# Performance work log

Hardware: AMD Instinct MI355X
Metric: run time of the kernel (lower is better)

## Reference

```python
import jax, jax.numpy as jnp
import numpy as np

B, N, DIM, H, DH = 4, 2048, 1024, 16, 64

def setup_inputs() -> dict:
    key = jax.random.key(0)
    k1, k2, k3 = jax.random.split(key, 3)
    x = jax.random.normal(k1, (B, N, DIM), dtype=jnp.float32)
    mask = jnp.ones((B, N), dtype=bool)
    w_qkv = jax.random.normal(k2, (DIM, 3 * H * DH), dtype=jnp.float32) * (DIM ** -0.5)
    w_out = jax.random.normal(k3, (H * DH, DIM), dtype=jnp.float32) * ((H * DH) ** -0.5)
    b_out = jnp.zeros((DIM,), dtype=jnp.float32)
    return {"x": x, "mask": mask, "w_qkv": w_qkv, "w_out": w_out, "b_out": b_out}

def reference(x, mask, w_qkv, w_out, b_out):
    b, n, _ = x.shape
    h, dh = H, DH
    scale = dh ** -0.5
    qkv = x @ w_qkv  # [b, n, 3*h*dh]
    q, k, v = jnp.split(qkv, 3, axis=-1)
    # [b, n, h*dh] -> [b, h, n, dh]
    reshape = lambda t: t.reshape(b, n, h, dh).transpose(0, 2, 1, 3)
    q, k, v = reshape(q) * scale, reshape(k), reshape(v)
    dots = jnp.einsum('bhid,bhjd->bhij', q, k)  # materialized N x N scores
    neg = -jnp.finfo(dots.dtype).max
    # key padding mask: [b, j] -> [b, 1, 1, j]
    dots = jnp.where(mask[:, None, None, :], dots, neg)
    # causal mask: mask out j > i
    causal = jnp.triu(jnp.ones((n, n), dtype=bool), k=1)
    dots = jnp.where(causal[None, None, :, :], neg, dots)
    attn = jax.nn.softmax(dots, axis=-1)
    out = jnp.einsum('bhij,bhjd->bhid', attn, v)
    out = out.transpose(0, 2, 1, 3).reshape(b, n, h * dh)
    return out @ w_out + b_out
```

## Files before the change

### kernel.cpp

```cpp
#include <hip/hip_runtime.h>

#define B_   4
#define N_   2048
#define DIM_ 1024
#define H_   16
#define DH_  64
#define NT   (B_ * N_)
#define PS   ((size_t)B_ * H_ * N_ * DH_)

typedef __bf16 bf16x8 __attribute__((ext_vector_type(8)));
typedef short  s16x4  __attribute__((ext_vector_type(4)));
typedef float  f32x4  __attribute__((ext_vector_type(4)));
typedef unsigned int   u32;
typedef unsigned int   u32x2 __attribute__((ext_vector_type(2)));
typedef unsigned short u16;

#define LOG2E 1.44269504088896f
#define QSCALE (0.125f * LOG2E)

__device__ __forceinline__ u16 f2bf(float f) {
  u32 u = __float_as_uint(f);
  u += 0x7FFFu + ((u >> 16) & 1u);
  return (u16)(u >> 16);
}

__device__ __forceinline__ u32 bfpack(float f0, float f1) {
  u32 a = __float_as_uint(f0) + 0x8000u;
  u32 b = __float_as_uint(f1) + 0x8000u;
  return __builtin_amdgcn_perm(b, a, 0x07060302);
}

__device__ __forceinline__ float fexp2(float x) {
  return __builtin_amdgcn_exp2f(x);
}

__device__ __forceinline__ f32x4 mfma32(bf16x8 a, bf16x8 b, f32x4 c) {
  return __builtin_amdgcn_mfma_f32_16x16x32_bf16(a, b, c, 0, 0, 0);
}
__device__ __forceinline__ f32x4 mfma16k(s16x4 a, s16x4 b, f32x4 c) {
  return __builtin_amdgcn_mfma_f32_16x16x16bf16_1k(a, b, c, 0, 0, 0);
}

__device__ __forceinline__ void gld16(const void* g, void* l) {
  __builtin_amdgcn_global_load_lds(
      (const __attribute__((address_space(1))) u32*)g,
      (__attribute__((address_space(3))) u32*)l, 16, 0, 0);
}

__global__ void convert_x_kernel(const float* __restrict__ x, u16* __restrict__ xb) {
  size_t i = ((size_t)blockIdx.x * 256 + threadIdx.x) * 8;
  float4 f0 = *(const float4*)(x + i);
  float4 f1 = *(const float4*)(x + i + 4);
  uint4 o;
  o.x = (u32)f2bf(f0.x) | ((u32)f2bf(f0.y) << 16);
  o.y = (u32)f2bf(f0.z) | ((u32)f2bf(f0.w) << 16);
  o.z = (u32)f2bf(f1.x) | ((u32)f2bf(f1.y) << 16);
  o.w = (u32)f2bf(f1.z) | ((u32)f2bf(f1.w) << 16);
  *(uint4*)(xb + i) = o;
}

__global__ void transpose_conv_kernel(const float* __restrict__ w, u16* __restrict__ wt,
                                      int K, int Ncols) {
  __shared__ u16 T[64 * 66];
  const int n0 = blockIdx.x * 64, k0 = blockIdx.y * 64;
  const int tid = threadIdx.x;
  const int r = tid >> 4, c4 = (tid & 15) * 4;
#pragma unroll
  for (int i = 0; i < 4; ++i) {
    int row = r + i * 16;
    float4 f = *(const float4*)(w + (size_t)(k0 + row) * Ncols + n0 + c4);
    u16* p = &T[row * 66 + c4];
    p[0] = f2bf(f.x); p[1] = f2bf(f.y); p[2] = f2bf(f.z); p[3] = f2bf(f.w);
  }
  __syncthreads();
  const int nr = tid >> 2, kc = (tid & 3) * 16;
  u32 p[8];
#pragma unroll
  for (int j = 0; j < 8; ++j)
    p[j] = (u32)T[(kc + 2 * j) * 66 + nr] | ((u32)T[(kc + 2 * j + 1) * 66 + nr] << 16);
  size_t dst = (size_t)(n0 + nr) * K + k0 + kc;
  *(uint4*)(wt + dst)     = make_uint4(p[0], p[1], p[2], p[3]);
  *(uint4*)(wt + dst + 8) = make_uint4(p[4], p[5], p[6], p[7]);
}

__global__ __launch_bounds__(256) void qkv_gemm_kernel(
    const u16* __restrict__ xb, const u16* __restrict__ wt,
    u16* __restrict__ q, u16* __restrict__ k, u16* __restrict__ vt) {
  __shared__ alignas(16) u16 As[128 * 64];
  __shared__ alignas(16) u16 Bs[128 * 64];
  const int tid = threadIdx.x, wave = tid >> 6, lane = tid & 63;
  const int quad = lane >> 4, l15 = lane & 15;
  const int wm = (wave >> 1) * 64, wn = (wave & 1) * 64;
  const int m0 = blockIdx.y * 128, n0 = blockIdx.x * 128;
  const int srow = lane >> 3;
  const int schunk = (lane & 7) ^ srow;

  f32x4 acc[4][4] = {};

  for (int kt = 0; kt < DIM_; kt += 64) {
    __syncthreads();
#pragma unroll
    for (int i = 0; i < 4; ++i) {
      int c = wave * 4 + i;
      int row = c * 8 + srow;
      gld16(xb + (size_t)(m0 + row) * DIM_ + kt + schunk * 8, As + c * 512);
      gld16(wt + (size_t)(n0 + row) * DIM_ + kt + schunk * 8, Bs + c * 512);
    }
    __syncthreads();
#pragma unroll
    for (int h = 0; h < 2; ++h) {
      bf16x8 af[4], bfr[4];
#pragma unroll
      for (int mi = 0; mi < 4; ++mi) {
        int row = wm + mi * 16 + l15;
        af[mi] = *(const bf16x8*)(As + row * 64 + (((quad + 4 * h) ^ (row & 7)) * 8));
      }
#pragma unroll
      for (int ni = 0; ni < 4; ++ni) {
        int row = wn + ni * 16 + l15;
        bfr[ni] = *(const bf16x8*)(Bs + row * 64 + (((quad + 4 * h) ^ (row & 7)) * 8));
      }
#pragma unroll
      for (int ni = 0; ni < 4; ++ni)
#pragma unroll
        for (int mi = 0; mi < 4; ++mi)
          acc[mi][ni] = mfma32(af[mi], bfr[ni], acc[mi][ni]);
    }
  }

#pragma unroll
  for (int ni = 0; ni < 4; ++ni) {
    int colg = n0 + wn + ni * 16 + l15;
    int part = colg >> 10, rem = colg & 1023;
    int hh = rem >> 6, d = rem & 63;
#pragma unroll
    for (int mi = 0; mi < 4; ++mi) {
      int row0 = m0 + wm + mi * 16 + quad * 4;
      int bb = row0 >> 11, nn0 = row0 & 2047;
      size_t bh = (size_t)(bb * H_ + hh);
      if (part == 0) {
#pragma unroll
        for (int r = 0; r < 4; ++r)
          q[(bh * N_ + nn0 + r) * DH_ + d] = f2bf(acc[mi][ni][r] * QSCALE);
      } else if (part == 1) {
#pragma unroll
        for (int r = 0; r < 4; ++r)
          k[(bh * N_ + nn0 + r) * DH_ + d] = f2bf(acc[mi][ni][r]);
      } else {
        u32 lo = bfpack(acc[mi][ni][0], acc[mi][ni][1]);
        u32 hi = bfpack(acc[mi][ni][2], acc[mi][ni][3]);
        *(uint2*)(vt + (bh * DH_ + d) * N_ + nn0) = make_uint2(lo, hi);
      }
    }
  }
}

__global__ __launch_bounds__(256) void attn_kernel(
    const u16* __restrict__ q, const u16* __restrict__ k,
    const u16* __restrict__ vt, u16* __restrict__ ctx) {
  __shared__ alignas(16) u16 Ks[128 * 64];
  __shared__ alignas(16) u16 Vs[64 * 128];
  const int tid = threadIdx.x, wave = tid >> 6, lane = tid & 63;
  const int quad = lane >> 4, l15 = lane & 15;
  const int head = blockIdx.x;
  const int p = blockIdx.y;
  const int hh = head & 15, bb = head >> 4;
  const int qtr0 = p, qtr1 = 31 - p;

  const size_t bhofs = (size_t)(bb * H_ + hh) << 17;
  const u16* qp = q + bhofs;
  const u16* kp = k + bhofs;
  const u16* vp = vt + bhofs;

  bf16x8 qf[2][2];
#pragma unroll
  for (int rg = 0; rg < 2; ++rg) {
    int rb = (rg ? qtr1 : qtr0) * 64 + wave * 16 + l15;
#pragma unroll
    for (int h = 0; h < 2; ++h)
      qf[rg][h] = *(const bf16x8*)(qp + (size_t)rb * 64 + h * 32 + quad * 8);
  }

  float m_s[2] = {-INFINITY, -INFINITY};
  float l_s[2] = {0.f, 0.f};
  f32x4 o[2][4] = {};

  const int ksrow = lane >> 3;
  const int kschunk = (lane & 7) ^ ksrow;
  const u16* kstage = kp + (size_t)ksrow * 64 + kschunk * 8;
  const int vsrow = lane >> 4;
  const u16* vstage0 = vp + (size_t)vsrow * N_;

  const int jmax = qtr1 >> 1;
  for (int jt = 0; jt <= jmax; ++jt) {
    __syncthreads();
#pragma unroll
    for (int i = 0; i < 4; ++i) {
      int c = wave * 4 + i;
      gld16(kstage + (size_t)(jt * 128 + c * 8) * 64, Ks + c * 512);
      int d = c * 4 + vsrow;
      int vch = (lane & 15) ^ (d & 7);
      gld16(vstage0 + (size_t)(c * 4) * N_ + jt * 128 + vch * 8, Vs + c * 512);
    }
    __syncthreads();

#pragma unroll
    for (int rg = 0; rg < 2; ++rg) {
      const int qt_rg = rg ? qtr1 : qtr0;
      if (jt > (qt_rg >> 1)) continue;

      const int rmin = qt_rg * 64 + wave * 16;
      const int kbmax = min(7, (rmin + 15 - jt * 128) >> 4);
      const bool diag = (jt == (qt_rg >> 1));

      f32x4 t[8];
#pragma unroll
      for (int kb = 0; kb < 8; ++kb) {
        if (kb <= kbmax) {
          int rk = kb * 16 + l15;
          bf16x8 k0 = *(const bf16x8*)(Ks + rk * 64 + ((quad ^ (rk & 7)) * 8));
          bf16x8 k1 = *(const bf16x8*)(Ks + rk * 64 + (((quad + 4) ^ (rk & 7)) * 8));
          f32x4 z = {};
          z = mfma32(k0, qf[rg][0], z);
          z = mfma32(k1, qf[rg][1], z);
          if (diag) {
            int rowl = ((qt_rg & 1) << 6) + wave * 16 + l15;
#pragma unroll
            for (int r = 0; r < 4; ++r)
              if (kb * 16 + quad * 4 + r > rowl) z[r] = -INFINITY;
          }
          t[kb] = z;
        }
      }
      float mx = -INFINITY;
#pragma unroll
      for (int kb = 0; kb < 8; ++kb)
        if (kb <= kbmax)
#pragma unroll
          for (int r = 0; r < 4; ++r) mx = fmaxf(mx, t[kb][r]);
      mx = fmaxf(mx, __shfl_xor(mx, 16));
      mx = fmaxf(mx, __shfl_xor(mx, 32));
      const float m_old = m_s[rg];
      const float mn = fmaxf(m_old, mx);
      if (__any(mx > m_old)) {
        float alpha = fexp2(m_old - mn);
        m_s[rg] = mn;
        l_s[rg] *= alpha;
#pragma unroll
        for (int db = 0; db < 4; ++db) o[rg][db] *= alpha;
      }
      float rs = 0.f;
#pragma unroll
      for (int kb = 0; kb < 8; ++kb) {
        if (kb <= kbmax) {
          float p0 = fexp2(t[kb][0] - mn), p1 = fexp2(t[kb][1] - mn);
          float p2 = fexp2(t[kb][2] - mn), p3 = fexp2(t[kb][3] - mn);
          rs += (p0 + p1) + (p2 + p3);
          u32x2 pp = {bfpack(p0, p1), bfpack(p2, p3)};
          s16x4 pbv = __builtin_bit_cast(s16x4, pp);
          int f = 2 * kb + (quad >> 1);
#pragma unroll
          for (int db = 0; db < 4; ++db) {
            int rv = db * 16 + l15;
            int ch = f ^ (rv & 7);
            s16x4 vf = *(const s16x4*)(Vs + rv * 128 + ch * 8 + (quad & 1) * 4);
            o[rg][db] = mfma16k(vf, pbv, o[rg][db]);
          }
        }
      }
      rs += __shfl_xor(rs, 16);
      rs += __shfl_xor(rs, 32);
      l_s[rg] += rs;
    }
  }

#pragma unroll
  for (int rg = 0; rg < 2; ++rg) {
    float inv = 1.0f / l_s[rg];
    int token = bb * N_ + (rg ? qtr1 : qtr0) * 64 + wave * 16 + l15;
#pragma unroll
    for (int db = 0; db < 4; ++db) {
      u32 lo = bfpack(o[rg][db][0] * inv, o[rg][db][1] * inv);
      u32 hi = bfpack(o[rg][db][2] * inv, o[rg][db][3] * inv);
      *(uint2*)(ctx + (size_t)token * DIM_ + hh * DH_ + db * 16 + quad * 4) =
          make_uint2(lo, hi);
    }
  }
}

__global__ __launch_bounds__(256) void out_gemm_kernel(
    const u16* __restrict__ cb, const u16* __restrict__ wt,
    const float* __restrict__ bias, float* __restrict__ out) {
  __shared__ alignas(16) u16 As[128 * 64];
  __shared__ alignas(16) u16 Bs[128 * 64];
  const int tid = threadIdx.x, wave = tid >> 6, lane = tid & 63;
  const int quad = lane >> 4, l15 = lane & 15;
  const int wm = (wave >> 1) * 64, wn = (wave & 1) * 64;
  const int m0 = blockIdx.y * 128, n0 = blockIdx.x * 128;
  const int srow = lane >> 3;
  const int schunk = (lane & 7) ^ srow;

  f32x4 acc[4][4] = {};

  for (int kt = 0; kt < DIM_; kt += 64) {
    __syncthreads();
#pragma unroll
    for (int i = 0; i < 4; ++i) {
      int c = wave * 4 + i;
      int row = c * 8 + srow;
      gld16(cb + (size_t)(m0 + row) * DIM_ + kt + schunk * 8, As + c * 512);
      gld16(wt + (size_t)(n0 + row) * DIM_ + kt + schunk * 8, Bs + c * 512);
    }
    __syncthreads();
#pragma unroll
    for (int h = 0; h < 2; ++h) {
      bf16x8 af[4], bfr[4];
#pragma unroll
      for (int mi = 0; mi < 4; ++mi) {
        int row = wm + mi * 16 + l15;
        af[mi] = *(const bf16x8*)(As + row * 64 + (((quad + 4 * h) ^ (row & 7)) * 8));
      }
#pragma unroll
      for (int ni = 0; ni < 4; ++ni) {
        int row = wn + ni * 16 + l15;
        bfr[ni] = *(const bf16x8*)(Bs + row * 64 + (((quad + 4 * h) ^ (row & 7)) * 8));
      }
#pragma unroll
      for (int ni = 0; ni < 4; ++ni)
#pragma unroll
        for (int mi = 0; mi < 4; ++mi)
          acc[mi][ni] = mfma32(af[mi], bfr[ni], acc[mi][ni]);
    }
  }

#pragma unroll
  for (int ni = 0; ni < 4; ++ni) {
    int col = n0 + wn + ni * 16 + l15;
    float bv = bias[col];
#pragma unroll
    for (int mi = 0; mi < 4; ++mi) {
      int row0 = m0 + wm + mi * 16 + quad * 4;
#pragma unroll
      for (int r = 0; r < 4; ++r)
        out[(size_t)(row0 + r) * DIM_ + col] = acc[mi][ni][r] + bv;
    }
  }
}

extern "C" void kernel_launch(void* const* d_in, const int* in_sizes, int n_in,
                              void* d_out, int out_size, void* d_ws, size_t ws_size,
                              hipStream_t stream) {
  (void)in_sizes; (void)n_in; (void)out_size; (void)ws_size;
  const float* x     = (const float*)d_in[0];
  const float* w_qkv = (const float*)d_in[2];
  const float* w_out = (const float*)d_in[3];
  const float* b_out = (const float*)d_in[4];
  float* out = (float*)d_out;

  u16* xb_ctx = (u16*)d_ws;
  u16* qw     = xb_ctx + (size_t)NT * DIM_;
  u16* kw     = qw + PS;
  u16* vw     = kw + PS;
  u16* wqkvT  = vw + PS;
  u16* woutT  = wqkvT + (size_t)3072 * 1024;

  convert_x_kernel<<<4096, 256, 0, stream>>>(x, xb_ctx);
  transpose_conv_kernel<<<dim3(48, 16), 256, 0, stream>>>(w_qkv, wqkvT, 1024, 3072);
  transpose_conv_kernel<<<dim3(16, 16), 256, 0, stream>>>(w_out, woutT, 1024, 1024);
  qkv_gemm_kernel<<<dim3(24, 64), 256, 0, stream>>>(xb_ctx, wqkvT, qw, kw, vw);
  attn_kernel<<<dim3(64, 16), 256, 0, stream>>>(qw, kw, vw, xb_ctx);
  out_gemm_kernel<<<dim3(8, 64), 256, 0, stream>>>(xb_ctx, woutT, b_out, out);
}
```

Baseline: 281.5 us.

## Split attention workgroup into two wave groups, one per paired query tile

The attention kernel now launches 512 threads per block. Eight waves are split into two groups of four, each handling one of the two causally paired query tiles (p and 31-p), instead of four waves looping over both tiles. Causal masking and softmax now run per 64-key half of each 128-key block, which skips masked 16-key sub-blocks at a finer granularity. The aim is more waves in flight, fewer registers per wave and less serial work per wave. The trade-off is that the group on the short tile sits idle through the later key blocks while still taking part in the K/V staging and barriers.

```diff
diff --git a/kernel.cpp b/kernel.cpp
--- a/kernel.cpp
+++ b/kernel.cpp
@@ -155,7 +155,7 @@
   }
 }
 
-__global__ __launch_bounds__(256) void attn_kernel(
+__global__ __launch_bounds__(512, 6) void attn_kernel(
     const u16* __restrict__ q, const u16* __restrict__ k,
     const u16* __restrict__ vt, u16* __restrict__ ctx) {
   __shared__ alignas(16) u16 Ks[128 * 64];
@@ -165,123 +165,119 @@
   const int head = blockIdx.x;
   const int p = blockIdx.y;
   const int hh = head & 15, bb = head >> 4;
-  const int qtr0 = p, qtr1 = 31 - p;
+  const int wgrp = wave >> 2, wsub = wave & 3;
+  const int qt = wgrp ? (31 - p) : p;
 
   const size_t bhofs = (size_t)(bb * H_ + hh) << 17;
   const u16* qp = q + bhofs;
   const u16* kp = k + bhofs;
   const u16* vp = vt + bhofs;
 
-  bf16x8 qf[2][2];
-#pragma unroll
-  for (int rg = 0; rg < 2; ++rg) {
-    int rb = (rg ? qtr1 : qtr0) * 64 + wave * 16 + l15;
-#pragma unroll
-    for (int h = 0; h < 2; ++h)
-      qf[rg][h] = *(const bf16x8*)(qp + (size_t)rb * 64 + h * 32 + quad * 8);
-  }
-
-  float m_s[2] = {-INFINITY, -INFINITY};
-  float l_s[2] = {0.f, 0.f};
-  f32x4 o[2][4] = {};
+  const int row = qt * 64 + wsub * 16 + l15;
+  const bf16x8 qf0 = *(const bf16x8*)(qp + (size_t)row * 64 + quad * 8);
+  const bf16x8 qf1 = *(const bf16x8*)(qp + (size_t)row * 64 + 32 + quad * 8);
+
+  float m_s = -INFINITY, l_s = 0.f;
+  f32x4 o[4] = {};
 
   const int ksrow = lane >> 3;
   const int kschunk = (lane & 7) ^ ksrow;
-  const u16* kstage = kp + (size_t)ksrow * 64 + kschunk * 8;
-  const int vsrow = lane >> 4;
-  const u16* vstage0 = vp + (size_t)vsrow * N_;
-
-  const int jmax = qtr1 >> 1;
+  const u16* kstage = kp + (size_t)(wave * 16 + ksrow) * 64 + kschunk * 8;
+  const int vd = wave * 8 + (lane >> 4);
+  const int vch = (lane & 15) ^ (lane >> 4);
+  const u16* vstage = vp + (size_t)vd * N_;
+
+  const int jmax = (31 - p) >> 1;
+  const int myjmax = qt >> 1;
+  const int rmin = qt * 64 + wsub * 16;
+
   for (int jt = 0; jt <= jmax; ++jt) {
     __syncthreads();
 #pragma unroll
-    for (int i = 0; i < 4; ++i) {
-      int c = wave * 4 + i;
-      gld16(kstage + (size_t)(jt * 128 + c * 8) * 64, Ks + c * 512);
-      int d = c * 4 + vsrow;
-      int vch = (lane & 15) ^ (d & 7);
-      gld16(vstage0 + (size_t)(c * 4) * N_ + jt * 128 + vch * 8, Vs + c * 512);
-    }
-    __syncthreads();
-
-#pragma unroll
-    for (int rg = 0; rg < 2; ++rg) {
-      const int qt_rg = rg ? qtr1 : qtr0;
-      if (jt > (qt_rg >> 1)) continue;
-
-      const int rmin = qt_rg * 64 + wave * 16;
-      const int kbmax = min(7, (rmin + 15 - jt * 128) >> 4);
-      const bool diag = (jt == (qt_rg >> 1));
-
-      f32x4 t[8];
-#pragma unroll
-      for (int kb = 0; kb < 8; ++kb) {
-        if (kb <= kbmax) {
-          int rk = kb * 16 + l15;
+    for (int i = 0; i < 2; ++i) {
+      int c = wave * 2 + i;
+      gld16(kstage + (size_t)(jt * 128 + i * 8) * 64, Ks + c * 512);
+      gld16(vstage + (size_t)(i * 4) * N_ + jt * 128 + (vch ^ (4 * i)) * 8,
+            Vs + c * 512);
+    }
+    __syncthreads();
+    if (jt > myjmax) continue;
+
+#pragma unroll
+    for (int half = 0; half < 2; ++half) {
+      const int keybase = jt * 128 + half * 64;
+      if (keybase > rmin + 15) break;
+      const int kbm = (rmin + 15 - keybase) >> 4;
+      const bool needmask = (keybase + 63 > rmin);
+      const int rowrel = row - keybase;
+
+      f32x4 t[4];
+#pragma unroll
+      for (int kb = 0; kb < 4; ++kb) {
+        if (kb <= kbm) {
+          int rk = half * 64 + kb * 16 + l15;
           bf16x8 k0 = *(const bf16x8*)(Ks + rk * 64 + ((quad ^ (rk & 7)) * 8));
           bf16x8 k1 = *(const bf16x8*)(Ks + rk * 64 + (((quad + 4) ^ (rk & 7)) * 8));
           f32x4 z = {};
-          z = mfma32(k0, qf[rg][0], z);
-          z = mfma32(k1, qf[rg][1], z);
-          if (diag) {
-            int rowl = ((qt_rg & 1) << 6) + wave * 16 + l15;
+          z = mfma32(k0, qf0, z);
+          z = mfma32(k1, qf1, z);
+          if (needmask) {
 #pragma unroll
             for (int r = 0; r < 4; ++r)
-              if (kb * 16 + quad * 4 + r > rowl) z[r] = -INFINITY;
+              if (kb * 16 + quad * 4 + r > rowrel) z[r] = -INFINITY;
           }
           t[kb] = z;
         }
       }
       float mx = -INFINITY;
 #pragma unroll
-      for (int kb = 0; kb < 8; ++kb)
-        if (kb <= kbmax)
+      for (int kb = 0; kb < 4; ++kb)
+        if (kb <= kbm)
 #pragma unroll
           for (int r = 0; r < 4; ++r) mx = fmaxf(mx, t[kb][r]);
       mx = fmaxf(mx, __shfl_xor(mx, 16));
       mx = fmaxf(mx, __shfl_xor(mx, 32));
-      const float m_old = m_s[rg];
+      const float m_old = m_s;
       const float mn = fmaxf(m_old, mx);
       if (__any(mx > m_old)) {
         float alpha = fexp2(m_old - mn);
-        m_s[rg] = mn;
-        l_s[rg] *= alpha;
-#pragma unroll
-        for (int db = 0; db < 4; ++db) o[rg][db] *= alpha;
+        m_s = mn;
+        l_s *= alpha;
+#pragma unroll
+        for (int db = 0; db < 4; ++db) o[db] *= alpha;
       }
       float rs = 0.f;
 #pragma unroll
-      for (int kb = 0; kb < 8; ++kb) {
-        if (kb <= kbmax) {
+      for (int kb = 0; kb < 4; ++kb) {
+        if (kb <= kbm) {
           float p0 = fexp2(t[kb][0] - mn), p1 = fexp2(t[kb][1] - mn);
           float p2 = fexp2(t[kb][2] - mn), p3 = fexp2(t[kb][3] - mn);
           rs += (p0 + p1) + (p2 + p3);
           u32x2 pp = {bfpack(p0, p1), bfpack(p2, p3)};
           s16x4 pbv = __builtin_bit_cast(s16x4, pp);
-          int f = 2 * kb + (quad >> 1);
+          int f = half * 8 + 2 * kb + (quad >> 1);
 #pragma unroll
           for (int db = 0; db < 4; ++db) {
             int rv = db * 16 + l15;
             int ch = f ^ (rv & 7);
             s16x4 vf = *(const s16x4*)(Vs + rv * 128 + ch * 8 + (quad & 1) * 4);
-            o[rg][db] = mfma16k(vf, pbv, o[rg][db]);
+            o[db] = mfma16k(vf, pbv, o[db]);
           }
         }
       }
       rs += __shfl_xor(rs, 16);
       rs += __shfl_xor(rs, 32);
-      l_s[rg] += rs;
-    }
-  }
-
-#pragma unroll
-  for (int rg = 0; rg < 2; ++rg) {
-    float inv = 1.0f / l_s[rg];
-    int token = bb * N_ + (rg ? qtr1 : qtr0) * 64 + wave * 16 + l15;
+      l_s += rs;
+    }
+  }
+
+  {
+    float inv = 1.0f / l_s;
+    int token = bb * N_ + row;
 #pragma unroll
     for (int db = 0; db < 4; ++db) {
-      u32 lo = bfpack(o[rg][db][0] * inv, o[rg][db][1] * inv);
-      u32 hi = bfpack(o[rg][db][2] * inv, o[rg][db][3] * inv);
+      u32 lo = bfpack(o[db][0] * inv, o[db][1] * inv);
+      u32 hi = bfpack(o[db][2] * inv, o[db][3] * inv);
       *(uint2*)(ctx + (size_t)token * DIM_ + hh * DH_ + db * 16 + quad * 4) =
           make_uint2(lo, hi);
     }
@@ -368,6 +364,6 @@
   transpose_conv_kernel<<<dim3(48, 16), 256, 0, stream>>>(w_qkv, wqkvT, 1024, 3072);
   transpose_conv_kernel<<<dim3(16, 16), 256, 0, stream>>>(w_out, woutT, 1024, 1024);
   qkv_gemm_kernel<<<dim3(24, 64), 256, 0, stream>>>(xb_ctx, wqkvT, qw, kw, vw);
-  attn_kernel<<<dim3(64, 16), 256, 0, stream>>>(qw, kw, vw, xb_ctx);
+  attn_kernel<<<dim3(64, 16), 512, 0, stream>>>(qw, kw, vw, xb_ctx);
   out_gemm_kernel<<<dim3(8, 64), 256, 0, stream>>>(xb_ctx, woutT, b_out, out);
 }
```

Result: no change. 279.7 us (-0.6%).
